# Optimization experiments

Hardware: AMD Instinct MI355X
Metric: run time of the kernel (lower is better)

Reference implementation:

```python
import jax, jax.numpy as jnp
from jax import lax
import numpy as np

LEVELS = 5
KSIZE = 45
SIGMA0 = 1.0
SIZE_ADDER = 0
SIGMA_MULT = 2.0


def _gauss1d(ksize, sigma):
    # Matches cv2.getGaussianKernel for sigma > 0: normalized Gaussian samples.
    x = np.arange(ksize, dtype=np.float64) - (ksize - 1) / 2.0
    g = np.exp(-(x * x) / (2.0 * sigma * sigma))
    return g / g.sum()


def _gauss2d(ksize, sigma):
    g1 = _gauss1d(ksize, sigma)
    return jnp.asarray(np.outer(g1, g1), dtype=jnp.float32)  # (k, k)


_KERNELS = [_gauss2d(KSIZE + SIZE_ADDER, SIGMA0 * SIGMA_MULT ** lvl) for lvl in range(LEVELS)]


def _blur(img, k2d):
    """Depthwise 2D Gaussian blur with replicate padding. img: (N,C,H,W), k2d: (k,k)."""
    C = img.shape[1]
    k = k2d.shape[0]
    pad = k // 2
    imgp = jnp.pad(img, ((0, 0), (0, 0), (pad, pad), (pad, pad)), mode='edge')
    kern = jnp.broadcast_to(k2d.astype(img.dtype), (C, 1, k, k))  # same filter per channel
    return lax.conv_general_dilated(
        imgp, kern, window_strides=(1, 1), padding='VALID',
        dimension_numbers=('NCHW', 'OIHW', 'NCHW'), feature_group_count=C)


def _blend(img0, img1, mask):
    # Fused Laplacian-stack build for img0/img1, Gaussian-stack for mask, and
    # lerp + sum-over-levels accumulation in a single pass over levels.
    cur0, cur1, curm = img0, img1, mask
    acc = jnp.zeros_like(img0)
    for lvl in range(LEVELS):
        if lvl < LEVELS - 1:
            k2d = _KERNELS[lvl]
            b0 = _blur(cur0, k2d)
            b1 = _blur(cur1, k2d)
            bm = _blur(curm, k2d)
            lap0 = cur0 - b0
            lap1 = cur1 - b1
            acc = acc + lap0 + curm * (lap1 - lap0)  # lerp(lap0, lap1, gauss_mask)
            cur0, cur1, curm = b0, b1, bm
        else:
            acc = acc + cur0 + curm * (cur1 - cur0)
    return acc


def setup_inputs() -> dict:
    key = jax.random.key(0)
    k0, k1, k2 = jax.random.split(key, 3)
    img0 = jax.random.normal(k0, (16, 3, 512, 512), dtype=jnp.float32)
    img1 = jax.random.normal(k1, (16, 3, 512, 512), dtype=jnp.float32)
    mask = jax.random.uniform(k2, (16, 1, 512, 512), dtype=jnp.float32)
    return {"img0": img0, "img1": img1, "mask": mask}


def reference(img0, img1, mask):
    return _blend(img0, img1, mask)
```

## Files before the change

### kernel.cpp

```cpp
#include <hip/hip_runtime.h>

#define PH 512
#define PW 512
#define PLANE (PH * PW)

enum { M_F0 = 0, M_MID = 1, M_MONLY = 2, M_LAST = 3 };

constexpr double cexp_pos(double z) {
  double term = 1.0, sum = 1.0;
  for (int k = 1; k < 160; ++k) {
    term *= z / (double)k;
    sum += term;
  }
  return sum;
}
template <int LVL, int R>
struct WTab {
  float w[2 * R + 1];
  constexpr WTab() : w{} {
    double sig = 1.0;
    for (int i = 0; i < LVL; ++i) sig *= 2.0;
    double g[2 * R + 1] = {};
    double s = 0.0;
    for (int t = 0; t <= 2 * R; ++t) {
      double x = (double)(t - R);
      g[t] = 1.0 / cexp_pos((x * x) / (2.0 * sig * sig));
      s += g[t];
    }
    for (int t = 0; t <= 2 * R; ++t) w[t] = (float)(g[t] / s);
  }
};

__device__ __forceinline__ int clampi(int v, int hi) {
  return v < 0 ? 0 : (v > hi ? hi : v);
}
__device__ __forceinline__ int swz(int bid, int nwg) {
  const int q = nwg >> 3;
  return (bid & 7) * q + (bid >> 3);
}
union HU { ushort u; _Float16 h; };
union BU { uint4 q; ushort u[8]; };
__device__ __forceinline__ float h2f(ushort s) {
  HU x; x.u = s; return (float)x.h;
}
__device__ __forceinline__ ushort f2h(float f) {
  HU x; x.h = (_Float16)f; return x.u;
}
__device__ __forceinline__ void q2f8(uint4 q, float* v) {
  BU b; b.q = q;
#pragma unroll
  for (int j = 0; j < 8; ++j) v[j] = h2f(b.u[j]);
}
__device__ __forceinline__ void sth8(ushort* __restrict__ p, const float* v) {
  BU b;
#pragma unroll
  for (int j = 0; j < 8; ++j) b.u[j] = f2h(v[j]);
  *(uint4*)p = b.q;
}
__device__ __forceinline__ void ff2f8(float4 a, float4 b, float* v) {
  v[0] = a.x; v[1] = a.y; v[2] = a.z; v[3] = a.w;
  v[4] = b.x; v[5] = b.y; v[6] = b.z; v[7] = b.w;
}
__device__ __forceinline__ void stf8(float* __restrict__ p, const float* v) {
  *(float4*)p = make_float4(v[0], v[1], v[2], v[3]);
  *(float4*)(p + 4) = make_float4(v[4], v[5], v[6], v[7]);
}

template <int LVL, int R, int MODE>
__global__ __launch_bounds__(512) void fused_lvl(
    const ushort* __restrict__ Sc, const ushort* __restrict__ Smk,
    const ushort* __restrict__ Gm4p, const float* __restrict__ in0,
    const float* __restrict__ in1, const float* __restrict__ inm,
    ushort* __restrict__ oS, ushort* __restrict__ oM,
    ushort* __restrict__ accP, float* __restrict__ outp, int cn3) {
  constexpr WTab<LVL, R> WT;
  constexpr int R8 = ((R + 7) / 8) * 8;
  constexpr int WW = 64 + 2 * R8;
  constexpr int WSTR = WW + 6;
  constexpr int VWIN = 64 + 2 * R;
  constexpr int NCH = WW / 8;
  __shared__ float Wb[VWIN * WSTR];
  __shared__ float Hb[VWIN * 67];

  const int bid = swz(blockIdx.x, gridDim.x);
  const int tid = threadIdx.x;
  const int p = bid >> 6, t = bid & 63;
  const int tx = t & 7;
  const int x0 = tx << 6, y0 = (t >> 3) << 6;
  const bool edge = (tx == 0) || (tx == 7);
  const int ey = tid >> 3, exq = (tid & 7) << 3;
  const size_t erow = (size_t)(y0 + ey) * PW + x0 + exq;

  const bool ismask = (MODE == M_MONLY) || (MODE != M_LAST && p >= cn3);
  const int pm = ismask ? ((MODE == M_MONLY) ? p : p - cn3) : 0;
  const int n = p / 3;

  uint4 qacc{}, qm{}, qm4{};
  float4 fi0a{}, fi0b{}, fmka{}, fmkb{};
  if (!ismask) {
    if (MODE == M_F0) {
      const float* p0 = in0 + (size_t)p * PLANE + erow;
      fi0a = ((const float4*)p0)[0];
      fi0b = ((const float4*)p0)[1];
      const float* pk = inm + (size_t)n * PLANE + erow;
      fmka = ((const float4*)pk)[0];
      fmkb = ((const float4*)pk)[1];
    } else {
      qacc = *(const uint4*)(accP + (size_t)p * PLANE + erow);
      qm = *(const uint4*)(Smk + (size_t)n * PLANE + erow);
      if (MODE == M_LAST)
        qm4 = *(const uint4*)(Gm4p + (size_t)n * PLANE + erow);
    }
  }

  {
    const int w = tid >> 6, rs = (tid >> 3) & 7, cs = tid & 7;
#pragma unroll
    for (int ro = 0; ro < VWIN; ro += 64) {
      const int row = ro + (w << 3) + rs;
#pragma unroll
      for (int cb = 0; cb < 2; ++cb) {
        const int ch = (cb << 3) + cs;
        if (row < VWIN && ch < NCH) {
          const int gy = clampi(y0 + row - R, PH - 1);
          const int gx = x0 - R8 + (ch << 3);
          float v[8];
          if (MODE == M_F0) {
            if (!ismask) {
              const float* r0 = in0 + (size_t)p * PLANE + (size_t)gy * PW;
              const float* r1 = in1 + (size_t)p * PLANE + (size_t)gy * PW;
              if (!edge || (gx >= 0 && gx <= PW - 8)) {
                float a[8], bb[8];
                ff2f8(((const float4*)(r0 + gx))[0],
                      ((const float4*)(r0 + gx))[1], a);
                ff2f8(((const float4*)(r1 + gx))[0],
                      ((const float4*)(r1 + gx))[1], bb);
#pragma unroll
                for (int j = 0; j < 8; ++j) v[j] = bb[j] - a[j];
              } else {
#pragma unroll
                for (int j = 0; j < 8; ++j) {
                  const int cx = clampi(gx + j, PW - 1);
                  v[j] = r1[cx] - r0[cx];
                }
              }
            } else {
              const float* rm = inm + (size_t)pm * PLANE + (size_t)gy * PW;
              if (!edge || (gx >= 0 && gx <= PW - 8)) {
                ff2f8(((const float4*)(rm + gx))[0],
                      ((const float4*)(rm + gx))[1], v);
              } else {
#pragma unroll
                for (int j = 0; j < 8; ++j) v[j] = rm[clampi(gx + j, PW - 1)];
              }
            }
          } else {
            const ushort* sp =
                (ismask ? Smk + (size_t)pm * PLANE : Sc + (size_t)p * PLANE) +
                (size_t)gy * PW;
            if (!edge || (gx >= 0 && gx <= PW - 8)) {
              q2f8(*(const uint4*)&sp[gx], v);
            } else {
#pragma unroll
              for (int j = 0; j < 8; ++j) v[j] = h2f(sp[clampi(gx + j, PW - 1)]);
            }
          }
          float* d = &Wb[row * WSTR + (ch << 3)];
#pragma unroll
          for (int k = 0; k < 4; ++k)
            *(float2*)&d[2 * k] = make_float2(v[2 * k], v[2 * k + 1]);
        }
      }
    }
  }
  __syncthreads();

  {
    const int cg = tid & 7;
    constexpr int basep = R8 - R;
#pragma unroll
    for (int ro = 0; ro < VWIN; ro += 64) {
      const int r = ro + (tid >> 3);
      if (r < VWIN) {
        const float* wr = &Wb[r * WSTR + basep + (cg << 3)];
        float a[8];
#pragma unroll
        for (int i = 0; i < 8; ++i) a[i] = 0.f;
#pragma unroll
        for (int j2 = 0; j2 < R + 4; ++j2) {
          const float2 v2 = *(const float2*)&wr[2 * j2];
          const int j0 = 2 * j2, j1 = 2 * j2 + 1;
#pragma unroll
          for (int i = 0; i < 8; ++i) {
            if (i <= j0 && j0 - i <= 2 * R)
              a[i] = fmaf(WT.w[j0 - i], v2.x, a[i]);
            if (i <= j1 && j1 - i <= 2 * R)
              a[i] = fmaf(WT.w[j1 - i], v2.y, a[i]);
          }
        }
        float* hr = &Hb[r * 67 + (cg << 3)];
#pragma unroll
        for (int i = 0; i < 8; ++i) hr[i] = a[i];
      }
    }
  }
  __syncthreads();

  const int lane = tid & 63, yg = tid >> 6;
  float b[8];
#pragma unroll
  for (int i = 0; i < 8; ++i) b[i] = 0.f;
#pragma unroll
  for (int j = 0; j < 2 * R + 8; ++j) {
    const float v = Hb[((yg << 3) + j) * 67 + lane];
#pragma unroll
    for (int i = 0; i < 8; ++i)
      if (i <= j && j - i <= 2 * R) b[i] = fmaf(WT.w[j - i], v, b[i]);
  }
  __syncthreads();
#pragma unroll
  for (int i = 0; i < 8; ++i) Hb[lane * 65 + (yg << 3) + i] = b[i];
  __syncthreads();
  float bs[8];
#pragma unroll
  for (int j = 0; j < 8; ++j) bs[j] = Hb[(exq + j) * 65 + ey];

  if (ismask) {
    sth8(oM + (size_t)pm * PLANE + erow, bs);
    return;
  }

  float D[8];
#pragma unroll
  for (int j = 0; j < 8; ++j) D[j] = Wb[(R + ey) * WSTR + R8 + exq + j];

  if (MODE == M_F0) {
    float i0v[8], mv[8], av[8];
    ff2f8(fi0a, fi0b, i0v);
    ff2f8(fmka, fmkb, mv);
#pragma unroll
    for (int j = 0; j < 8; ++j) av[j] = i0v[j] + mv[j] * (D[j] - bs[j]);
    sth8(accP + (size_t)p * PLANE + erow, av);
    sth8(oS + (size_t)p * PLANE + erow, bs);
  } else if (MODE == M_MID) {
    float av[8], mv[8];
    q2f8(qacc, av);
    q2f8(qm, mv);
#pragma unroll
    for (int j = 0; j < 8; ++j) av[j] += mv[j] * (D[j] - bs[j]);
    sth8(accP + (size_t)p * PLANE + erow, av);
    sth8(oS + (size_t)p * PLANE + erow, bs);
  } else {
    float av[8], m3[8], m4[8], o[8];
    q2f8(qacc, av);
    q2f8(qm, m3);
    q2f8(qm4, m4);
#pragma unroll
    for (int j = 0; j < 8; ++j)
      o[j] = av[j] + m3[j] * (D[j] - bs[j]) + m4[j] * bs[j];
    stf8(outp + (size_t)p * PLANE + erow, o);
  }
}

extern "C" void kernel_launch(void* const* d_in, const int* in_sizes, int n_in,
                              void* d_out, int out_size, void* d_ws,
                              size_t ws_size, hipStream_t stream) {
  const float* img0 = (const float*)d_in[0];
  const float* img1 = (const float*)d_in[1];
  const float* mask = (const float*)d_in[2];
  float* out = (float*)d_out;

  const int NTOT = 16;
  const size_t perImg = (size_t)11 * PLANE * sizeof(ushort);
  int CN = 16;
  while (CN > 1 && (size_t)CN * perImg > ws_size) CN >>= 1;

  for (int s = 0; s < NTOT; s += CN) {
    ushort* SA = (ushort*)d_ws;
    ushort* SB = SA + (size_t)4 * CN * PLANE;
    ushort* acc = SB + (size_t)4 * CN * PLANE;
    ushort* SAm = SA + (size_t)3 * CN * PLANE;
    ushort* SBm = SB + (size_t)3 * CN * PLANE;

    const float* in0 = img0 + (size_t)s * 3 * PLANE;
    const float* in1 = img1 + (size_t)s * 3 * PLANE;
    const float* inm = mask + (size_t)s * PLANE;
    float* o = out + (size_t)s * 3 * PLANE;

    const int cn3 = 3 * CN;
    const dim3 blk(512);
    const int gAll = 4 * CN * 64, gD = 3 * CN * 64, gM = CN * 64;
    const ushort* nb = nullptr;
    const float* nf = nullptr;

    hipLaunchKernelGGL((fused_lvl<0, 6, M_F0>), dim3(gAll), blk, 0, stream, nb,
                       nb, nb, in0, in1, inm, SA, SAm, acc, (float*)nullptr,
                       cn3);
    hipLaunchKernelGGL((fused_lvl<1, 10, M_MID>), dim3(gAll), blk, 0, stream,
                       SA, SAm, nb, nf, nf, nf, SB, SBm, acc, (float*)nullptr,
                       cn3);
    hipLaunchKernelGGL((fused_lvl<2, 18, M_MID>), dim3(gAll), blk, 0, stream,
                       SB, SBm, nb, nf, nf, nf, SA, SAm, acc, (float*)nullptr,
                       cn3);
    hipLaunchKernelGGL((fused_lvl<3, 22, M_MONLY>), dim3(gM), blk, 0, stream,
                       nb, SAm, nb, nf, nf, nf, (ushort*)nullptr, SBm,
                       (ushort*)nullptr, (float*)nullptr, cn3);
    hipLaunchKernelGGL((fused_lvl<3, 22, M_LAST>), dim3(gD), blk, 0, stream, SA,
                       SAm, SBm, nf, nf, nf, (ushort*)nullptr,
                       (ushort*)nullptr, acc, o, cn3);
  }
}
```

Before: 239.7 us.

## Parameterize tile height and use shorter tiles for larger-radius levels

Adds a template parameter for output tile height: 32 rows for the first three levels and 16 rows for level 3, keeping 64-wide tiles and 512 threads. Loading and horizontal-pass loops become generic strided job loops, and the epilogue switches to four elements per thread, with threads beyond the tile idling. Shorter tiles cut shared memory per block and raise the number of blocks, improving occupancy and parallelism. In exchange the vertical halo is a larger share of each tile, so there is more redundant global reading and horizontal filtering.

Result: slower. 302.4 us (+26.1%).

```diff
diff --git a/kernel.cpp b/kernel.cpp
--- a/kernel.cpp
+++ b/kernel.cpp
@@ -40,6 +40,7 @@
 }
 union HU { ushort u; _Float16 h; };
 union BU { uint4 q; ushort u[8]; };
+union BU2 { uint2 q; ushort u[4]; };
 __device__ __forceinline__ float h2f(ushort s) {
   HU x; x.u = s; return (float)x.h;
 }
@@ -51,22 +52,23 @@
 #pragma unroll
   for (int j = 0; j < 8; ++j) v[j] = h2f(b.u[j]);
 }
-__device__ __forceinline__ void sth8(ushort* __restrict__ p, const float* v) {
-  BU b;
-#pragma unroll
-  for (int j = 0; j < 8; ++j) b.u[j] = f2h(v[j]);
-  *(uint4*)p = b.q;
+__device__ __forceinline__ void q2f4(uint2 q, float* v) {
+  BU2 b; b.q = q;
+#pragma unroll
+  for (int j = 0; j < 4; ++j) v[j] = h2f(b.u[j]);
+}
+__device__ __forceinline__ void sth4(ushort* __restrict__ p, const float* v) {
+  BU2 b;
+#pragma unroll
+  for (int j = 0; j < 4; ++j) b.u[j] = f2h(v[j]);
+  *(uint2*)p = b.q;
 }
 __device__ __forceinline__ void ff2f8(float4 a, float4 b, float* v) {
   v[0] = a.x; v[1] = a.y; v[2] = a.z; v[3] = a.w;
   v[4] = b.x; v[5] = b.y; v[6] = b.z; v[7] = b.w;
 }
-__device__ __forceinline__ void stf8(float* __restrict__ p, const float* v) {
-  *(float4*)p = make_float4(v[0], v[1], v[2], v[3]);
-  *(float4*)(p + 4) = make_float4(v[4], v[5], v[6], v[7]);
-}
-
-template <int LVL, int R, int MODE>
+
+template <int LVL, int R, int TH, int MODE>
 __global__ __launch_bounds__(512) void fused_lvl(
     const ushort* __restrict__ Sc, const ushort* __restrict__ Smk,
     const ushort* __restrict__ Gm4p, const float* __restrict__ in0,
@@ -77,188 +79,176 @@
   constexpr int R8 = ((R + 7) / 8) * 8;
   constexpr int WW = 64 + 2 * R8;
   constexpr int WSTR = WW + 6;
-  constexpr int VWIN = 64 + 2 * R;
+  constexpr int VWIN = TH + 2 * R;
   constexpr int NCH = WW / 8;
+  constexpr int NJOBS = VWIN * NCH;
+  constexpr int NHJ = VWIN * 8;
+  constexpr int RPT = TH / 8;
+  constexpr int TSTR = TH + 1;
+  constexpr int NTILE = 8 * (PH / TH);
+  constexpr int HBF = (VWIN * 67 > 64 * TSTR) ? VWIN * 67 : 64 * TSTR;
   __shared__ float Wb[VWIN * WSTR];
-  __shared__ float Hb[VWIN * 67];
+  __shared__ float Hb[HBF];
 
   const int bid = swz(blockIdx.x, gridDim.x);
   const int tid = threadIdx.x;
-  const int p = bid >> 6, t = bid & 63;
+  const int p = bid / NTILE, t = bid & (NTILE - 1);
   const int tx = t & 7;
-  const int x0 = tx << 6, y0 = (t >> 3) << 6;
+  const int x0 = tx << 6, y0 = (t >> 3) * TH;
   const bool edge = (tx == 0) || (tx == 7);
-  const int ey = tid >> 3, exq = (tid & 7) << 3;
-  const size_t erow = (size_t)(y0 + ey) * PW + x0 + exq;
+  const bool epi = tid < TH * 16;
+  const int ey = tid >> 4, ex4 = (tid & 15) << 2;
+  const size_t erow = (size_t)(y0 + ey) * PW + x0 + ex4;
 
   const bool ismask = (MODE == M_MONLY) || (MODE != M_LAST && p >= cn3);
   const int pm = ismask ? ((MODE == M_MONLY) ? p : p - cn3) : 0;
   const int n = p / 3;
 
-  uint4 qacc{}, qm{}, qm4{};
-  float4 fi0a{}, fi0b{}, fmka{}, fmkb{};
-  if (!ismask) {
+  uint2 qacc{}, qm{}, qm4{};
+  float4 fi0{}, fmk{};
+  if (!ismask && epi) {
     if (MODE == M_F0) {
-      const float* p0 = in0 + (size_t)p * PLANE + erow;
-      fi0a = ((const float4*)p0)[0];
-      fi0b = ((const float4*)p0)[1];
-      const float* pk = inm + (size_t)n * PLANE + erow;
-      fmka = ((const float4*)pk)[0];
-      fmkb = ((const float4*)pk)[1];
+      fi0 = *(const float4*)(in0 + (size_t)p * PLANE + erow);
+      fmk = *(const float4*)(inm + (size_t)n * PLANE + erow);
     } else {
-      qacc = *(const uint4*)(accP + (size_t)p * PLANE + erow);
-      qm = *(const uint4*)(Smk + (size_t)n * PLANE + erow);
+      qacc = *(const uint2*)(accP + (size_t)p * PLANE + erow);
+      qm = *(const uint2*)(Smk + (size_t)n * PLANE + erow);
       if (MODE == M_LAST)
-        qm4 = *(const uint4*)(Gm4p + (size_t)n * PLANE + erow);
+        qm4 = *(const uint2*)(Gm4p + (size_t)n * PLANE + erow);
     }
   }
 
-  {
-    const int w = tid >> 6, rs = (tid >> 3) & 7, cs = tid & 7;
-#pragma unroll
-    for (int ro = 0; ro < VWIN; ro += 64) {
-      const int row = ro + (w << 3) + rs;
-#pragma unroll
-      for (int cb = 0; cb < 2; ++cb) {
-        const int ch = (cb << 3) + cs;
-        if (row < VWIN && ch < NCH) {
-          const int gy = clampi(y0 + row - R, PH - 1);
-          const int gx = x0 - R8 + (ch << 3);
-          float v[8];
-          if (MODE == M_F0) {
-            if (!ismask) {
-              const float* r0 = in0 + (size_t)p * PLANE + (size_t)gy * PW;
-              const float* r1 = in1 + (size_t)p * PLANE + (size_t)gy * PW;
-              if (!edge || (gx >= 0 && gx <= PW - 8)) {
-                float a[8], bb[8];
-                ff2f8(((const float4*)(r0 + gx))[0],
-                      ((const float4*)(r0 + gx))[1], a);
-                ff2f8(((const float4*)(r1 + gx))[0],
-                      ((const float4*)(r1 + gx))[1], bb);
-#pragma unroll
-                for (int j = 0; j < 8; ++j) v[j] = bb[j] - a[j];
-              } else {
-#pragma unroll
-                for (int j = 0; j < 8; ++j) {
-                  const int cx = clampi(gx + j, PW - 1);
-                  v[j] = r1[cx] - r0[cx];
-                }
-              }
-            } else {
-              const float* rm = inm + (size_t)pm * PLANE + (size_t)gy * PW;
-              if (!edge || (gx >= 0 && gx <= PW - 8)) {
-                ff2f8(((const float4*)(rm + gx))[0],
-                      ((const float4*)(rm + gx))[1], v);
-              } else {
-#pragma unroll
-                for (int j = 0; j < 8; ++j) v[j] = rm[clampi(gx + j, PW - 1)];
-              }
-            }
-          } else {
-            const ushort* sp =
-                (ismask ? Smk + (size_t)pm * PLANE : Sc + (size_t)p * PLANE) +
-                (size_t)gy * PW;
-            if (!edge || (gx >= 0 && gx <= PW - 8)) {
-              q2f8(*(const uint4*)&sp[gx], v);
-            } else {
-#pragma unroll
-              for (int j = 0; j < 8; ++j) v[j] = h2f(sp[clampi(gx + j, PW - 1)]);
-            }
+  for (int j0 = tid; j0 < NJOBS; j0 += 512) {
+    const int row = j0 / NCH, ch = j0 % NCH;
+    const int gy = clampi(y0 + row - R, PH - 1);
+    const int gx = x0 - R8 + (ch << 3);
+    float v[8];
+    if (MODE == M_F0) {
+      if (!ismask) {
+        const float* r0 = in0 + (size_t)p * PLANE + (size_t)gy * PW;
+        const float* r1 = in1 + (size_t)p * PLANE + (size_t)gy * PW;
+        if (!edge || (gx >= 0 && gx <= PW - 8)) {
+          float a[8], bb[8];
+          ff2f8(((const float4*)(r0 + gx))[0], ((const float4*)(r0 + gx))[1], a);
+          ff2f8(((const float4*)(r1 + gx))[0], ((const float4*)(r1 + gx))[1], bb);
+#pragma unroll
+          for (int j = 0; j < 8; ++j) v[j] = bb[j] - a[j];
+        } else {
+#pragma unroll
+          for (int j = 0; j < 8; ++j) {
+            const int cx = clampi(gx + j, PW - 1);
+            v[j] = r1[cx] - r0[cx];
           }
-          float* d = &Wb[row * WSTR + (ch << 3)];
-#pragma unroll
-          for (int k = 0; k < 4; ++k)
-            *(float2*)&d[2 * k] = make_float2(v[2 * k], v[2 * k + 1]);
+        }
+      } else {
+        const float* rm = inm + (size_t)pm * PLANE + (size_t)gy * PW;
+        if (!edge || (gx >= 0 && gx <= PW - 8)) {
+          ff2f8(((const float4*)(rm + gx))[0], ((const float4*)(rm + gx))[1], v);
+        } else {
+#pragma unroll
+          for (int j = 0; j < 8; ++j) v[j] = rm[clampi(gx + j, PW - 1)];
         }
       }
-    }
-  }
-  __syncthreads();
-
-  {
-    const int cg = tid & 7;
-    constexpr int basep = R8 - R;
-#pragma unroll
-    for (int ro = 0; ro < VWIN; ro += 64) {
-      const int r = ro + (tid >> 3);
-      if (r < VWIN) {
-        const float* wr = &Wb[r * WSTR + basep + (cg << 3)];
-        float a[8];
-#pragma unroll
-        for (int i = 0; i < 8; ++i) a[i] = 0.f;
-#pragma unroll
-        for (int j2 = 0; j2 < R + 4; ++j2) {
-          const float2 v2 = *(const float2*)&wr[2 * j2];
-          const int j0 = 2 * j2, j1 = 2 * j2 + 1;
-#pragma unroll
-          for (int i = 0; i < 8; ++i) {
-            if (i <= j0 && j0 - i <= 2 * R)
-              a[i] = fmaf(WT.w[j0 - i], v2.x, a[i]);
-            if (i <= j1 && j1 - i <= 2 * R)
-              a[i] = fmaf(WT.w[j1 - i], v2.y, a[i]);
-          }
-        }
-        float* hr = &Hb[r * 67 + (cg << 3)];
-#pragma unroll
-        for (int i = 0; i < 8; ++i) hr[i] = a[i];
+    } else {
+      const ushort* sp =
+          (ismask ? Smk + (size_t)pm * PLANE : Sc + (size_t)p * PLANE) +
+          (size_t)gy * PW;
+      if (!edge || (gx >= 0 && gx <= PW - 8)) {
+        q2f8(*(const uint4*)&sp[gx], v);
+      } else {
+#pragma unroll
+        for (int j = 0; j < 8; ++j) v[j] = h2f(sp[clampi(gx + j, PW - 1)]);
       }
     }
+    float* d = &Wb[row * WSTR + (ch << 3)];
+#pragma unroll
+    for (int k = 0; k < 4; ++k)
+      *(float2*)&d[2 * k] = make_float2(v[2 * k], v[2 * k + 1]);
   }
   __syncthreads();
 
+  for (int j0 = tid; j0 < NHJ; j0 += 512) {
+    const int r = j0 >> 3, cg = j0 & 7;
+    constexpr int basep = R8 - R;
+    const float* wr = &Wb[r * WSTR + basep + (cg << 3)];
+    float a[8];
+#pragma unroll
+    for (int i = 0; i < 8; ++i) a[i] = 0.f;
+#pragma unroll
+    for (int j2 = 0; j2 < R + 4; ++j2) {
+      const float2 v2 = *(const float2*)&wr[2 * j2];
+      const int j0e = 2 * j2, j1e = 2 * j2 + 1;
+#pragma unroll
+      for (int i = 0; i < 8; ++i) {
+        if (i <= j0e && j0e - i <= 2 * R) a[i] = fmaf(WT.w[j0e - i], v2.x, a[i]);
+        if (i <= j1e && j1e - i <= 2 * R) a[i] = fmaf(WT.w[j1e - i], v2.y, a[i]);
+      }
+    }
+    float* hr = &Hb[r * 67 + (cg << 3)];
+#pragma unroll
+    for (int i = 0; i < 8; ++i) hr[i] = a[i];
+  }
+  __syncthreads();
+
   const int lane = tid & 63, yg = tid >> 6;
-  float b[8];
-#pragma unroll
-  for (int i = 0; i < 8; ++i) b[i] = 0.f;
-#pragma unroll
-  for (int j = 0; j < 2 * R + 8; ++j) {
-    const float v = Hb[((yg << 3) + j) * 67 + lane];
-#pragma unroll
-    for (int i = 0; i < 8; ++i)
+  float b[RPT];
+#pragma unroll
+  for (int i = 0; i < RPT; ++i) b[i] = 0.f;
+#pragma unroll
+  for (int j = 0; j < 2 * R + RPT; ++j) {
+    const float v = Hb[(yg * RPT + j) * 67 + lane];
+#pragma unroll
+    for (int i = 0; i < RPT; ++i)
       if (i <= j && j - i <= 2 * R) b[i] = fmaf(WT.w[j - i], v, b[i]);
   }
   __syncthreads();
 #pragma unroll
-  for (int i = 0; i < 8; ++i) Hb[lane * 65 + (yg << 3) + i] = b[i];
+  for (int i = 0; i < RPT; ++i) Hb[lane * TSTR + yg * RPT + i] = b[i];
   __syncthreads();
-  float bs[8];
-#pragma unroll
-  for (int j = 0; j < 8; ++j) bs[j] = Hb[(exq + j) * 65 + ey];
+
+  if (!epi) return;
+  float bs[4];
+#pragma unroll
+  for (int j = 0; j < 4; ++j) bs[j] = Hb[(ex4 + j) * TSTR + ey];
 
   if (ismask) {
-    sth8(oM + (size_t)pm * PLANE + erow, bs);
+    sth4(oM + (size_t)pm * PLANE + erow, bs);
     return;
   }
 
-  float D[8];
-#pragma unroll
-  for (int j = 0; j < 8; ++j) D[j] = Wb[(R + ey) * WSTR + R8 + exq + j];
+  float D[4];
+  {
+    const float* dp = &Wb[(R + ey) * WSTR + R8 + ex4];
+    const float2 d0 = *(const float2*)dp;
+    const float2 d1 = *(const float2*)(dp + 2);
+    D[0] = d0.x; D[1] = d0.y; D[2] = d1.x; D[3] = d1.y;
+  }
 
   if (MODE == M_F0) {
-    float i0v[8], mv[8], av[8];
-    ff2f8(fi0a, fi0b, i0v);
-    ff2f8(fmka, fmkb, mv);
-#pragma unroll
-    for (int j = 0; j < 8; ++j) av[j] = i0v[j] + mv[j] * (D[j] - bs[j]);
-    sth8(accP + (size_t)p * PLANE + erow, av);
-    sth8(oS + (size_t)p * PLANE + erow, bs);
+    float av[4];
+    av[0] = fi0.x + fmk.x * (D[0] - bs[0]);
+    av[1] = fi0.y + fmk.y * (D[1] - bs[1]);
+    av[2] = fi0.z + fmk.z * (D[2] - bs[2]);
+    av[3] = fi0.w + fmk.w * (D[3] - bs[3]);
+    sth4(accP + (size_t)p * PLANE + erow, av);
+    sth4(oS + (size_t)p * PLANE + erow, bs);
   } else if (MODE == M_MID) {
-    float av[8], mv[8];
-    q2f8(qacc, av);
-    q2f8(qm, mv);
-#pragma unroll
-    for (int j = 0; j < 8; ++j) av[j] += mv[j] * (D[j] - bs[j]);
-    sth8(accP + (size_t)p * PLANE + erow, av);
-    sth8(oS + (size_t)p * PLANE + erow, bs);
+    float av[4], mv[4];
+    q2f4(qacc, av);
+    q2f4(qm, mv);
+#pragma unroll
+    for (int j = 0; j < 4; ++j) av[j] += mv[j] * (D[j] - bs[j]);
+    sth4(accP + (size_t)p * PLANE + erow, av);
+    sth4(oS + (size_t)p * PLANE + erow, bs);
   } else {
-    float av[8], m3[8], m4[8], o[8];
-    q2f8(qacc, av);
-    q2f8(qm, m3);
-    q2f8(qm4, m4);
-#pragma unroll
-    for (int j = 0; j < 8; ++j)
+    float av[4], m3[4], m4[4], o[4];
+    q2f4(qacc, av);
+    q2f4(qm, m3);
+    q2f4(qm4, m4);
+#pragma unroll
+    for (int j = 0; j < 4; ++j)
       o[j] = av[j] + m3[j] * (D[j] - bs[j]) + m4[j] * bs[j];
-    stf8(outp + (size_t)p * PLANE + erow, o);
+    *(float4*)(outp + (size_t)p * PLANE + erow) = make_float4(o[0], o[1], o[2], o[3]);
   }
 }
 
@@ -289,24 +279,26 @@
 
     const int cn3 = 3 * CN;
     const dim3 blk(512);
-    const int gAll = 4 * CN * 64, gD = 3 * CN * 64, gM = CN * 64;
+    const int g32 = 4 * CN * 128;
+    const int gM16 = CN * 256;
+    const int gD16 = 3 * CN * 256;
     const ushort* nb = nullptr;
     const float* nf = nullptr;
 
-    hipLaunchKernelGGL((fused_lvl<0, 6, M_F0>), dim3(gAll), blk, 0, stream, nb,
-                       nb, nb, in0, in1, inm, SA, SAm, acc, (float*)nullptr,
+    hipLaunchKernelGGL((fused_lvl<0, 6, 32, M_F0>), dim3(g32), blk, 0, stream,
+                       nb, nb, nb, in0, in1, inm, SA, SAm, acc, (float*)nullptr,
                        cn3);
-    hipLaunchKernelGGL((fused_lvl<1, 10, M_MID>), dim3(gAll), blk, 0, stream,
+    hipLaunchKernelGGL((fused_lvl<1, 10, 32, M_MID>), dim3(g32), blk, 0, stream,
                        SA, SAm, nb, nf, nf, nf, SB, SBm, acc, (float*)nullptr,
                        cn3);
-    hipLaunchKernelGGL((fused_lvl<2, 18, M_MID>), dim3(gAll), blk, 0, stream,
+    hipLaunchKernelGGL((fused_lvl<2, 18, 32, M_MID>), dim3(g32), blk, 0, stream,
                        SB, SBm, nb, nf, nf, nf, SA, SAm, acc, (float*)nullptr,
                        cn3);
-    hipLaunchKernelGGL((fused_lvl<3, 22, M_MONLY>), dim3(gM), blk, 0, stream,
-                       nb, SAm, nb, nf, nf, nf, (ushort*)nullptr, SBm,
+    hipLaunchKernelGGL((fused_lvl<3, 22, 16, M_MONLY>), dim3(gM16), blk, 0,
+                       stream, nb, SAm, nb, nf, nf, nf, (ushort*)nullptr, SBm,
                        (ushort*)nullptr, (float*)nullptr, cn3);
-    hipLaunchKernelGGL((fused_lvl<3, 22, M_LAST>), dim3(gD), blk, 0, stream, SA,
-                       SAm, SBm, nf, nf, nf, (ushort*)nullptr,
+    hipLaunchKernelGGL((fused_lvl<3, 22, 16, M_LAST>), dim3(gD16), blk, 0,
+                       stream, SA, SAm, SBm, nf, nf, nf, (ushort*)nullptr,
                        (ushort*)nullptr, acc, o, cn3);
   }
 }
```
